# Optimization experiments

Hardware: AMD Instinct MI355X
Metric: run time of the kernel (lower is better)

Reference implementation:

```python
import jax, jax.numpy as jnp
import numpy as np

EPS = 1e-06

def _feature_map(x):
    # elu(x) + 1 -> strictly positive feature map
    return jax.nn.elu(x) + 1.0

def setup_inputs() -> dict:
    key = jax.random.key(0)
    kq, kk, kv = jax.random.split(key, 3)
    B, H, N, D = 1, 16, 2048, 64
    Q = jax.random.normal(kq, (B, H, N, D), dtype=jnp.float32)
    K = jax.random.normal(kk, (B, H, N, D), dtype=jnp.float32)
    V = jax.random.normal(kv, (B, H, N, D), dtype=jnp.float32)
    return {"Q": Q, "K": K, "V": V, "causal": 1}

def reference(Q, K, V, causal):
    Qf = _feature_map(Q)  # (B,H,N,D)
    Kf = _feature_map(K)  # (B,H,N,D)
    if causal:
        # prefix sums of per-position outer products K_m V_m^T  -> (B,H,N,D,Dv)
        KV_prefix = jnp.cumsum(Kf[..., :, None] * V[..., None, :], axis=2)
        Kf_prefix = jnp.cumsum(Kf, axis=2)  # (B,H,N,D)
        num = jnp.einsum('bhnd,bhnde->bhne', Qf, KV_prefix)
        den = jnp.einsum('bhnd,bhnd->bhn', Qf, Kf_prefix)[..., None]
        return num / (den + EPS)
    else:
        KV = jnp.einsum('bhnd,bhne->bhde', Kf, V)            # (B,H,D,Dv)
        num = jnp.einsum('bhnd,bhde->bhne', Qf, KV)          # (B,H,N,Dv)
        den = jnp.einsum('bhnd,bhd->bhn', Qf, Kf.sum(axis=2))[..., None]
        return num / (den + EPS)
```

## Files before the change

### kernel.cpp

```cpp
#include <hip/hip_runtime.h>

#define Hh   16
#define Nn   2048
#define Dd   64
#define DVv  64
#define Ll   64
#define Cc   (Nn / Ll)
#define HCc  (Hh * Cc)
#define EPSf 1e-6f
#define LDP  72

typedef __attribute__((ext_vector_type(8))) __bf16 bf16x8;
typedef __attribute__((ext_vector_type(4))) __bf16 bf16x4;
typedef __attribute__((ext_vector_type(4))) float  f32x4;

__device__ __forceinline__ float fmap(float x) {
    return x > 0.0f ? (x + 1.0f) : __expf(x);
}
__device__ __forceinline__ __bf16 tobf(float x) { return (__bf16)x; }

__global__ __launch_bounds__(256) void k_chunk_sums(
    const float* __restrict__ Kg, const float* __restrict__ Vg,
    __bf16* __restrict__ SwsT, float* __restrict__ zws)
{
    __shared__ __align__(16) __bf16 sKT[Dd][LDP];
    __shared__ __align__(16) __bf16 sVT[80][LDP];
    const int t  = threadIdx.x;
    const int hc = blockIdx.x;
    const float4* K4 = (const float4*)(Kg + (size_t)hc * (Ll * Dd));
    const float4* V4 = (const float4*)(Vg + (size_t)hc * (Ll * DVv));
    for (int i = t; i < (Ll * Dd) / 4; i += 256) {
        float4 k4 = K4[i];
        float4 v4 = V4[i];
        const int m  = i >> 4;
        const int c0 = (i & 15) * 4;
        sKT[c0 + 0][m] = tobf(fmap(k4.x));
        sKT[c0 + 1][m] = tobf(fmap(k4.y));
        sKT[c0 + 2][m] = tobf(fmap(k4.z));
        sKT[c0 + 3][m] = tobf(fmap(k4.w));
        sVT[c0 + 0][m] = tobf(v4.x);
        sVT[c0 + 1][m] = tobf(v4.y);
        sVT[c0 + 2][m] = tobf(v4.z);
        sVT[c0 + 3][m] = tobf(v4.w);
    }
    for (int i = t; i < 16 * LDP; i += 256) {
        const int r = i / LDP, c = i % LDP;
        sVT[64 + r][c] = (r == 0) ? (__bf16)1.0f : (__bf16)0.0f;
    }
    __syncthreads();

    const int lane = t & 63, wv = t >> 6;
    const int col = lane & 15, quad = lane >> 4;
    __bf16* So = SwsT + (size_t)hc * (Dd * DVv);
    for (int et = 0; et < 5; ++et) {
        f32x4 acc = {0.f, 0.f, 0.f, 0.f};
#pragma unroll
        for (int ks = 0; ks < 2; ++ks) {
            bf16x8 a = *(const bf16x8*)&sKT[wv * 16 + col][ks * 32 + quad * 8];
            bf16x8 b = *(const bf16x8*)&sVT[et * 16 + col][ks * 32 + quad * 8];
            acc = __builtin_amdgcn_mfma_f32_16x16x32_bf16(a, b, acc, 0, 0, 0);
        }
        if (et < 4) {
            const int e = et * 16 + col;
            const int d = wv * 16 + quad * 4;
            bf16x4 s4 = { tobf(acc[0]), tobf(acc[1]), tobf(acc[2]), tobf(acc[3]) };
            *(bf16x4*)&So[e * Dd + d] = s4;
        } else if (col == 0) {
#pragma unroll
            for (int j = 0; j < 4; ++j)
                zws[hc * Dd + wv * 16 + quad * 4 + j] = acc[j];
        }
    }
}

__global__ __launch_bounds__(256) void k_prefix(
    __bf16* __restrict__ SwsT, float* __restrict__ zws)
{
    const int b = blockIdx.x, t = threadIdx.x;
    if (b < 32) {
        const int gid = b * 256 + t;
        const int h   = gid >> 9;
        const int sl  = gid & 511;
        __bf16* base = SwsT + ((size_t)h * Cc) * (Dd * DVv) + sl * 8;
        float run[8];
#pragma unroll
        for (int j = 0; j < 8; ++j) run[j] = 0.0f;
#pragma unroll
        for (int cb = 0; cb < 4; ++cb) {
            bf16x8 v[8];
#pragma unroll
            for (int k = 0; k < 8; ++k)
                v[k] = *(const bf16x8*)(base + (size_t)(cb * 8 + k) * (Dd * DVv));
#pragma unroll
            for (int k = 0; k < 8; ++k) {
                bf16x8 o;
#pragma unroll
                for (int j = 0; j < 8; ++j) {
                    o[j] = tobf(run[j]);
                    run[j] += (float)v[k][j];
                }
                *(bf16x8*)(base + (size_t)(cb * 8 + k) * (Dd * DVv)) = o;
            }
        }
    } else {
        const int gid = (b - 32) * 256 + t;
        const int h = gid >> 6, d = gid & 63;
        float* zb = zws + (h * Cc) * Dd + d;
        float run = 0.0f;
#pragma unroll
        for (int cb = 0; cb < 4; ++cb) {
            float v[8];
#pragma unroll
            for (int k = 0; k < 8; ++k) v[k] = zb[(cb * 8 + k) * Dd];
#pragma unroll
            for (int k = 0; k < 8; ++k) {
                zb[(cb * 8 + k) * Dd] = run;
                run += v[k];
            }
        }
    }
}

__global__ __launch_bounds__(256) void k_output(
    const float* __restrict__ Qg, const float* __restrict__ Kg,
    const float* __restrict__ Vg, const __bf16* __restrict__ SwsT,
    const float* __restrict__ zws, float* __restrict__ Og)
{
    __shared__ __align__(16) __bf16 aQ[Ll][LDP];
    __shared__ __align__(16) __bf16 aK[Ll][LDP];
    __shared__ __align__(16) __bf16 sW[Ll][LDP];
    __shared__ __align__(16) __bf16 bV[80][LDP];
    __shared__ __align__(16) __bf16 bS[80][LDP];
    const int t  = threadIdx.x;
    const int hc = blockIdx.x;
    const int lane = t & 63, wv = t >> 6;
    const int col = lane & 15, quad = lane >> 4;

    {
        const float4* Q4 = (const float4*)(Qg + (size_t)hc * (Ll * Dd));
        const float4* K4 = (const float4*)(Kg + (size_t)hc * (Ll * Dd));
        const float4* V4 = (const float4*)(Vg + (size_t)hc * (Ll * DVv));
        for (int i = t; i < (Ll * Dd) / 4; i += 256) {
            float4 q4 = Q4[i];
            float4 k4 = K4[i];
            float4 v4 = V4[i];
            const int m  = i >> 4;
            const int c0 = (i & 15) * 4;
            bf16x4 qv = { tobf(fmap(q4.x)), tobf(fmap(q4.y)), tobf(fmap(q4.z)), tobf(fmap(q4.w)) };
            bf16x4 kv = { tobf(fmap(k4.x)), tobf(fmap(k4.y)), tobf(fmap(k4.z)), tobf(fmap(k4.w)) };
            *(bf16x4*)&aQ[m][c0] = qv;
            *(bf16x4*)&aK[m][c0] = kv;
            bV[c0 + 0][m] = tobf(v4.x);
            bV[c0 + 1][m] = tobf(v4.y);
            bV[c0 + 2][m] = tobf(v4.z);
            bV[c0 + 3][m] = tobf(v4.w);
        }
        for (int i = t; i < 16 * LDP; i += 256) {
            const int r = i / LDP, cc = i % LDP;
            bV[64 + r][cc] = (r == 0) ? (__bf16)1.0f : (__bf16)0.0f;
        }
    }

    {
        const __bf16* Sp = SwsT + (size_t)hc * (Dd * DVv);
        for (int i = t; i < (Dd * DVv) / 8; i += 256) {
            bf16x8 s = *(const bf16x8*)(Sp + i * 8);
            const int e = i >> 3, d0 = (i & 7) * 8;
            *(bf16x8*)&bS[e][d0] = s;
        }
        if (t < Dd) bS[64][t] = tobf(zws[hc * Dd + t]);
        for (int i = t; i < 16 * LDP; i += 256) {
            const int r = i / LDP, cc = i % LDP;
            if (!(r == 0 && cc < Dd)) bS[64 + r][cc] = (__bf16)0.0f;
        }
    }
    __syncthreads();

#pragma unroll 1
    for (int mt = 0; mt < 4; ++mt) {
        f32x4 wacc = {0.f, 0.f, 0.f, 0.f};
#pragma unroll
        for (int ks = 0; ks < 2; ++ks) {
            bf16x8 a = *(const bf16x8*)&aQ[wv * 16 + col][ks * 32 + quad * 8];
            bf16x8 b = *(const bf16x8*)&aK[mt * 16 + col][ks * 32 + quad * 8];
            wacc = __builtin_amdgcn_mfma_f32_16x16x32_bf16(a, b, wacc, 0, 0, 0);
        }
#pragma unroll
        for (int j = 0; j < 4; ++j) {
            const int n = wv * 16 + quad * 4 + j;
            const int m = mt * 16 + col;
            sW[n][m] = tobf(m <= n ? wacc[j] : 0.0f);
        }
    }
    __syncthreads();

    f32x4 accs[5];
#pragma unroll 1
    for (int et = 0; et < 5; ++et) {
        f32x4 acc = {0.f, 0.f, 0.f, 0.f};
#pragma unroll
        for (int ks = 0; ks < 2; ++ks) {
            bf16x8 a = *(const bf16x8*)&sW[wv * 16 + col][ks * 32 + quad * 8];
            bf16x8 b = *(const bf16x8*)&bV[et * 16 + col][ks * 32 + quad * 8];
            acc = __builtin_amdgcn_mfma_f32_16x16x32_bf16(a, b, acc, 0, 0, 0);
        }
#pragma unroll
        for (int ks = 0; ks < 2; ++ks) {
            bf16x8 a = *(const bf16x8*)&aQ[wv * 16 + col][ks * 32 + quad * 8];
            bf16x8 b = *(const bf16x8*)&bS[et * 16 + col][ks * 32 + quad * 8];
            acc = __builtin_amdgcn_mfma_f32_16x16x32_bf16(a, b, acc, 0, 0, 0);
        }
        accs[et] = acc;
    }
    float dn[4];
#pragma unroll
    for (int j = 0; j < 4; ++j) dn[j] = __shfl(accs[4][j], lane & 48);

    float* Oc = Og + (size_t)hc * (Ll * DVv);
#pragma unroll
    for (int et = 0; et < 4; ++et) {
#pragma unroll
        for (int j = 0; j < 4; ++j) {
            const int n = wv * 16 + quad * 4 + j;
            Oc[n * DVv + et * 16 + col] = accs[et][j] / (dn[j] + EPSf);
        }
    }
}

extern "C" void kernel_launch(void* const* d_in, const int* in_sizes, int n_in,
                              void* d_out, int out_size, void* d_ws, size_t ws_size,
                              hipStream_t stream) {
    const float* Q = (const float*)d_in[0];
    const float* K = (const float*)d_in[1];
    const float* V = (const float*)d_in[2];
    __bf16* SwsT = (__bf16*)d_ws;
    float*  zws  = (float*)((char*)d_ws + (size_t)HCc * Dd * DVv * sizeof(__bf16));
    float* out = (float*)d_out;

    k_chunk_sums<<<HCc, 256, 0, stream>>>(K, V, SwsT, zws);
    k_prefix<<<36, 256, 0, stream>>>(SwsT, zws);
    k_output<<<HCc, 256, 0, stream>>>(Q, K, V, SwsT, zws, out);
}
```

Baseline: 88.94 us.

## Cache bf16 feature-mapped K/V in workspace and widen prefix-scan parallelism

The chunk-sum kernel now also writes the feature-mapped K and the V values as bf16 into workspace, so the output kernel reads half-size bf16 data instead of recomputing from fp32 inputs. The prefix kernel is relaunched with many more 64-thread blocks, each scanning 4 columns across all chunks, to raise parallelism in that latency-bound step. A barrier after the sW write is dropped because each wave reads only the rows it wrote. The trade-off is extra global writes in the first kernel and more workspace use.

```diff
diff --git a/kernel.cpp b/kernel.cpp
--- a/kernel.cpp
+++ b/kernel.cpp
@@ -21,7 +21,8 @@
 
 __global__ __launch_bounds__(256) void k_chunk_sums(
     const float* __restrict__ Kg, const float* __restrict__ Vg,
-    __bf16* __restrict__ SwsT, float* __restrict__ zws)
+    __bf16* __restrict__ SwsT, float* __restrict__ zws,
+    __bf16* __restrict__ Kfg, __bf16* __restrict__ Vbg)
 {
     __shared__ __align__(16) __bf16 sKT[Dd][LDP];
     __shared__ __align__(16) __bf16 sVT[80][LDP];
@@ -29,19 +30,25 @@
     const int hc = blockIdx.x;
     const float4* K4 = (const float4*)(Kg + (size_t)hc * (Ll * Dd));
     const float4* V4 = (const float4*)(Vg + (size_t)hc * (Ll * DVv));
+    __bf16* Kfo = Kfg + (size_t)hc * (Ll * Dd);
+    __bf16* Vbo = Vbg + (size_t)hc * (Ll * DVv);
     for (int i = t; i < (Ll * Dd) / 4; i += 256) {
         float4 k4 = K4[i];
         float4 v4 = V4[i];
         const int m  = i >> 4;
         const int c0 = (i & 15) * 4;
-        sKT[c0 + 0][m] = tobf(fmap(k4.x));
-        sKT[c0 + 1][m] = tobf(fmap(k4.y));
-        sKT[c0 + 2][m] = tobf(fmap(k4.z));
-        sKT[c0 + 3][m] = tobf(fmap(k4.w));
-        sVT[c0 + 0][m] = tobf(v4.x);
-        sVT[c0 + 1][m] = tobf(v4.y);
-        sVT[c0 + 2][m] = tobf(v4.z);
-        sVT[c0 + 3][m] = tobf(v4.w);
+        bf16x4 kv = { tobf(fmap(k4.x)), tobf(fmap(k4.y)), tobf(fmap(k4.z)), tobf(fmap(k4.w)) };
+        bf16x4 vv = { tobf(v4.x), tobf(v4.y), tobf(v4.z), tobf(v4.w) };
+        *(bf16x4*)&Kfo[m * Dd + c0]  = kv;
+        *(bf16x4*)&Vbo[m * DVv + c0] = vv;
+        sKT[c0 + 0][m] = kv[0];
+        sKT[c0 + 1][m] = kv[1];
+        sKT[c0 + 2][m] = kv[2];
+        sKT[c0 + 3][m] = kv[3];
+        sVT[c0 + 0][m] = vv[0];
+        sVT[c0 + 1][m] = vv[1];
+        sVT[c0 + 2][m] = vv[2];
+        sVT[c0 + 3][m] = vv[3];
     }
     for (int i = t; i < 16 * LDP; i += 256) {
         const int r = i / LDP, c = i % LDP;
@@ -73,57 +80,48 @@
     }
 }
 
-__global__ __launch_bounds__(256) void k_prefix(
+__global__ __launch_bounds__(64) void k_prefix(
     __bf16* __restrict__ SwsT, float* __restrict__ zws)
 {
     const int b = blockIdx.x, t = threadIdx.x;
-    if (b < 32) {
-        const int gid = b * 256 + t;
-        const int h   = gid >> 9;
-        const int sl  = gid & 511;
-        __bf16* base = SwsT + ((size_t)h * Cc) * (Dd * DVv) + sl * 8;
-        float run[8];
-#pragma unroll
-        for (int j = 0; j < 8; ++j) run[j] = 0.0f;
-#pragma unroll
-        for (int cb = 0; cb < 4; ++cb) {
-            bf16x8 v[8];
-#pragma unroll
-            for (int k = 0; k < 8; ++k)
-                v[k] = *(const bf16x8*)(base + (size_t)(cb * 8 + k) * (Dd * DVv));
-#pragma unroll
-            for (int k = 0; k < 8; ++k) {
-                bf16x8 o;
-#pragma unroll
-                for (int j = 0; j < 8; ++j) {
-                    o[j] = tobf(run[j]);
-                    run[j] += (float)v[k][j];
-                }
-                *(bf16x8*)(base + (size_t)(cb * 8 + k) * (Dd * DVv)) = o;
-            }
+    if (b < 256) {
+        const int gid = b * 64 + t;
+        const int h   = gid >> 10;
+        const int sl  = gid & 1023;
+        __bf16* base = SwsT + ((size_t)h * Cc) * (Dd * DVv) + sl * 4;
+        bf16x4 v[Cc];
+#pragma unroll
+        for (int k = 0; k < Cc; ++k)
+            v[k] = *(const bf16x4*)(base + (size_t)k * (Dd * DVv));
+        float r0 = 0.f, r1 = 0.f, r2 = 0.f, r3 = 0.f;
+#pragma unroll
+        for (int k = 0; k < Cc; ++k) {
+            bf16x4 o = { tobf(r0), tobf(r1), tobf(r2), tobf(r3) };
+            *(bf16x4*)(base + (size_t)k * (Dd * DVv)) = o;
+            r0 += (float)v[k][0];
+            r1 += (float)v[k][1];
+            r2 += (float)v[k][2];
+            r3 += (float)v[k][3];
         }
     } else {
-        const int gid = (b - 32) * 256 + t;
+        const int gid = (b - 256) * 64 + t;
         const int h = gid >> 6, d = gid & 63;
-        float* zb = zws + (h * Cc) * Dd + d;
-        float run = 0.0f;
-#pragma unroll
-        for (int cb = 0; cb < 4; ++cb) {
-            float v[8];
-#pragma unroll
-            for (int k = 0; k < 8; ++k) v[k] = zb[(cb * 8 + k) * Dd];
-#pragma unroll
-            for (int k = 0; k < 8; ++k) {
-                zb[(cb * 8 + k) * Dd] = run;
-                run += v[k];
-            }
+        float* zb = zws + (size_t)(h * Cc) * Dd + d;
+        float v[Cc];
+#pragma unroll
+        for (int k = 0; k < Cc; ++k) v[k] = zb[(size_t)k * Dd];
+        float run = 0.f;
+#pragma unroll
+        for (int k = 0; k < Cc; ++k) {
+            zb[(size_t)k * Dd] = run;
+            run += v[k];
         }
     }
 }
 
 __global__ __launch_bounds__(256) void k_output(
-    const float* __restrict__ Qg, const float* __restrict__ Kg,
-    const float* __restrict__ Vg, const __bf16* __restrict__ SwsT,
+    const float* __restrict__ Qg, const __bf16* __restrict__ Kfg,
+    const __bf16* __restrict__ Vbg, const __bf16* __restrict__ SwsT,
     const float* __restrict__ zws, float* __restrict__ Og)
 {
     __shared__ __align__(16) __bf16 aQ[Ll][LDP];
@@ -138,22 +136,23 @@
 
     {
         const float4* Q4 = (const float4*)(Qg + (size_t)hc * (Ll * Dd));
-        const float4* K4 = (const float4*)(Kg + (size_t)hc * (Ll * Dd));
-        const float4* V4 = (const float4*)(Vg + (size_t)hc * (Ll * DVv));
         for (int i = t; i < (Ll * Dd) / 4; i += 256) {
             float4 q4 = Q4[i];
-            float4 k4 = K4[i];
-            float4 v4 = V4[i];
             const int m  = i >> 4;
             const int c0 = (i & 15) * 4;
             bf16x4 qv = { tobf(fmap(q4.x)), tobf(fmap(q4.y)), tobf(fmap(q4.z)), tobf(fmap(q4.w)) };
-            bf16x4 kv = { tobf(fmap(k4.x)), tobf(fmap(k4.y)), tobf(fmap(k4.z)), tobf(fmap(k4.w)) };
             *(bf16x4*)&aQ[m][c0] = qv;
-            *(bf16x4*)&aK[m][c0] = kv;
-            bV[c0 + 0][m] = tobf(v4.x);
-            bV[c0 + 1][m] = tobf(v4.y);
-            bV[c0 + 2][m] = tobf(v4.z);
-            bV[c0 + 3][m] = tobf(v4.w);
+        }
+        const __bf16* Kf = Kfg + (size_t)hc * (Ll * Dd);
+        const __bf16* Vb = Vbg + (size_t)hc * (Ll * DVv);
+        for (int i = t; i < (Ll * Dd) / 8; i += 256) {
+            bf16x8 k8 = *(const bf16x8*)(Kf + i * 8);
+            bf16x8 v8 = *(const bf16x8*)(Vb + i * 8);
+            const int m  = i >> 3;
+            const int c0 = (i & 7) * 8;
+            *(bf16x8*)&aK[m][c0] = k8;
+#pragma unroll
+            for (int j = 0; j < 8; ++j) bV[c0 + j][m] = v8[j];
         }
         for (int i = t; i < 16 * LDP; i += 256) {
             const int r = i / LDP, cc = i % LDP;
@@ -192,7 +191,6 @@
             sW[n][m] = tobf(m <= n ? wacc[j] : 0.0f);
         }
     }
-    __syncthreads();
 
     f32x4 accs[5];
 #pragma unroll 1
@@ -233,11 +231,16 @@
     const float* Q = (const float*)d_in[0];
     const float* K = (const float*)d_in[1];
     const float* V = (const float*)d_in[2];
-    __bf16* SwsT = (__bf16*)d_ws;
-    float*  zws  = (float*)((char*)d_ws + (size_t)HCc * Dd * DVv * sizeof(__bf16));
+    char* ws = (char*)d_ws;
+    const size_t szS = (size_t)HCc * Dd * DVv * sizeof(__bf16);
+    const size_t szZ = (size_t)HCc * Dd * sizeof(float);
+    __bf16* SwsT = (__bf16*)ws;
+    float*  zws  = (float*)(ws + szS);
+    __bf16* Kfws = (__bf16*)(ws + szS + szZ);
+    __bf16* Vbws = Kfws + (size_t)HCc * Ll * Dd;
     float* out = (float*)d_out;
 
-    k_chunk_sums<<<HCc, 256, 0, stream>>>(K, V, SwsT, zws);
-    k_prefix<<<36, 256, 0, stream>>>(SwsT, zws);
-    k_output<<<HCc, 256, 0, stream>>>(Q, K, V, SwsT, zws, out);
-}
+    k_chunk_sums<<<HCc, 256, 0, stream>>>(K, V, SwsT, zws, Kfws, Vbws);
+    k_prefix<<<272, 64, 0, stream>>>(SwsT, zws);
+    k_output<<<HCc, 256, 0, stream>>>(Q, Kfws, Vbws, SwsT, zws, out);
+}
```

Result: no change. 89.36 us (+0.5%).
